# Kernel tuning notes

Measured on AMD Instinct MI355X. Metric: run time of the kernel, lower is better.

Reference implementation:

```python
import jax, jax.numpy as jnp
import numpy as np

G = 4        # split_group
H = 64       # hidden_size_t = 256 // 4 (causal -> //1)
I = 64       # input_size_t  = 256 // 4
EPS = 1e-5


def _lstm(x, W_ih, W_hh, b):
    """Grouped unidirectional LSTM, PyTorch gate order (i,f,g,o).
    x: (G,B,T,I); W_ih: (G,4H,I); W_hh: (G,4H,H); b: (G,4H) -> (G,B,T,H)"""
    g, bsz, t, _ = x.shape
    h_dim = W_hh.shape[-1]
    # precompute input projections for all timesteps
    xp = jnp.einsum('gbti,gki->gbtk', x, W_ih) + b[:, None, None, :]  # (G,B,T,4H)
    xp = jnp.moveaxis(xp, 2, 0)  # (T,G,B,4H)

    def step(carry, xt):
        h, c = carry
        gates = xt + jnp.einsum('gbh,gkh->gbk', h, W_hh)
        i_g, f_g, g_g, o_g = jnp.split(gates, 4, axis=-1)
        i_g = jax.nn.sigmoid(i_g)
        f_g = jax.nn.sigmoid(f_g)
        g_g = jnp.tanh(g_g)
        o_g = jax.nn.sigmoid(o_g)
        c = f_g * c + i_g * g_g
        h = o_g * jnp.tanh(c)
        return (h, c), h

    h0 = jnp.zeros((g, bsz, h_dim), x.dtype)
    _, hs = jax.lax.scan(step, (h0, h0), xp)  # hs: (T,G,B,H)
    return jnp.moveaxis(hs, 0, 2)  # (G,B,T,H)


def _bn(x, gamma, beta):
    """BatchNorm1d (training stats) over (B,T) per feature. x: (B,T,F)"""
    mean = x.mean(axis=(0, 1))
    var = x.var(axis=(0, 1))
    return (x - mean) * jax.lax.rsqrt(var + EPS) * gamma + beta


def setup_inputs() -> dict:
    key = jax.random.key(0)
    ks = jax.random.split(key, 12)
    s = 0.1
    F = G * H
    return {
        'inpt': jax.random.normal(ks[0], (32, 1000, 256), jnp.float32),
        'W_ih1': jax.random.normal(ks[1], (G, 4 * H, I), jnp.float32) * s,
        'W_hh1': jax.random.normal(ks[2], (G, 4 * H, H), jnp.float32) * s,
        'b1': jax.random.normal(ks[3], (G, 4 * H), jnp.float32) * s,
        'W_ih2': jax.random.normal(ks[4], (G, 4 * H, H), jnp.float32) * s,
        'W_hh2': jax.random.normal(ks[5], (G, 4 * H, H), jnp.float32) * s,
        'b2': jax.random.normal(ks[6], (G, 4 * H), jnp.float32) * s,
        'gamma1': jnp.ones((F,), jnp.float32) + jax.random.normal(ks[7], (F,)) * 0.01,
        'beta1': jax.random.normal(ks[8], (F,), jnp.float32) * 0.01,
        'gamma2': jnp.ones((F,), jnp.float32) + jax.random.normal(ks[9], (F,)) * 0.01,
        'beta2': jax.random.normal(ks[10], (F,), jnp.float32) * 0.01,
    }


def reference(inpt, W_ih1, W_hh1, b1, W_ih2, W_hh2, b2, gamma1, beta1, gamma2, beta2):
    B, T, F = inpt.shape
    # chunk along features -> (G,B,T,I)
    xg = jnp.transpose(inpt.reshape(B, T, G, I), (2, 0, 1, 3))
    y1 = _lstm(xg, W_ih1, W_hh1, b1)  # (G,B,T,H)
    # torch.stack(dim=-1) + flatten: feature index = h*G + g (interleaved)
    x = jnp.transpose(y1, (1, 2, 3, 0)).reshape(B, T, H * G)
    x = _bn(x, gamma1, beta1)
    # chunk again into G contiguous groups of size H
    xg2 = jnp.transpose(x.reshape(B, T, G, H), (2, 0, 1, 3))
    y2 = _lstm(xg2, W_ih2, W_hh2, b2)  # (G,B,T,H)
    # torch.cat(dim=-1): contiguous groups
    x = jnp.transpose(y2, (1, 2, 0, 3)).reshape(B, T, G * H)
    x = _bn(x, gamma2, beta2)
    return x
```

## Files before the change

### kernel.cpp

```cpp
#include <hip/hip_runtime.h>
#include <math.h>

#define G 4
#define H 64
#define T 1000
#define B 32
#define ROWS (B*T)

typedef _Float16 f16;
typedef _Float16 f16x2 __attribute__((ext_vector_type(2)));

#if defined(__has_builtin)
#if __has_builtin(__builtin_amdgcn_fdot2)
#define HAVE_FDOT2 1
#endif
#endif

__device__ __forceinline__ float dot2(f16x2 a, f16x2 b, float c) {
#ifdef HAVE_FDOT2
    return __builtin_amdgcn_fdot2(a, b, c, false);
#else
    return fmaf((float)a[0], (float)b[0], fmaf((float)a[1], (float)b[1], c));
#endif
}

__device__ __forceinline__ float sigm(float x) {
    return 1.f / (1.f + __expf(-x));
}
__device__ __forceinline__ float tanh_f(float x) {
    return 2.f / (1.f + __expf(-2.f * x)) - 1.f;
}

template<int LAYER>
__device__ void rec_wave4(const float* __restrict__ xp,
                          const float* __restrict__ Whh,
                          float* __restrict__ out,
                          float* __restrict__ stateh, float* __restrict__ statec,
                          float* __restrict__ sums,
                          int t0, int t1, int tcmax)
{
    __builtin_amdgcn_s_setprio(1);
    __shared__ __align__(16) _Float16 hx[4][64];
    const int wv = threadIdx.x >> 6;
    const int c  = threadIdx.x & 63;
    const int sq = blockIdx.x * 4 + wv;
    const int g = sq >> 5, b = sq & 31;

    f16x2 wpk[4][32];
    #pragma unroll
    for (int gt = 0; gt < 4; ++gt) {
        const float2* wp = (const float2*)&Whh[(size_t)((g * 256 + gt * 64 + c) << 6)];
        #pragma unroll
        for (int k = 0; k < 32; ++k) {
            float2 v = wp[k];
            f16x2 r; r[0] = (f16)v.x; r[1] = (f16)v.y;
            wpk[gt][k] = r;
        }
    }

    f16x2 hpk[32];
    float cst;
    if (t0 == 0) {
        #pragma unroll
        for (int k = 0; k < 32; ++k) { f16x2 z; z[0] = (f16)0.f; z[1] = (f16)0.f; hpk[k] = z; }
        cst = 0.f;
    } else {
        const float2* sh = (const float2*)&stateh[sq * 64];
        #pragma unroll
        for (int k = 0; k < 32; ++k) {
            float2 v = sh[k];
            f16x2 r; r[0] = (f16)v.x; r[1] = (f16)v.y;
            hpk[k] = r;
        }
        cst = statec[sq * 64 + c];
    }

    const float* xpb = xp + (size_t)sq * tcmax * 256;
    float p[4][4];
    #pragma unroll
    for (int j = 0; j < 4; ++j) {
        int tp = t0 + j; if (tp > t1 - 1) tp = t1 - 1;
        #pragma unroll
        for (int gt = 0; gt < 4; ++gt)
            p[j][gt] = xpb[(size_t)(tp - t0) * 256 + gt * 64 + c];
    }

    float st_s = 0.f, st_ss = 0.f, hl = 0.f;
    const int nsteps = t1 - t0;
    for (int s4 = 0; s4 < nsteps; s4 += 4) {
        #pragma unroll
        for (int j = 0; j < 4; ++j) {
            float pre[4];
            #pragma unroll
            for (int gt = 0; gt < 4; ++gt) {
                float a0 = 0.f, a1 = 0.f;
                #pragma unroll
                for (int k = 0; k < 32; k += 2) {
                    a0 = dot2(wpk[gt][k],     hpk[k],     a0);
                    a1 = dot2(wpk[gt][k + 1], hpk[k + 1], a1);
                }
                pre[gt] = (a0 + a1) + p[j][gt];
            }
            {
                int tp = t0 + s4 + j + 4; if (tp > t1 - 1) tp = t1 - 1;
                #pragma unroll
                for (int gt = 0; gt < 4; ++gt)
                    p[j][gt] = xpb[(size_t)(tp - t0) * 256 + gt * 64 + c];
            }
            float ig = sigm(pre[0]);
            float fg = sigm(pre[1]);
            float gg = tanh_f(pre[2]);
            float og = sigm(pre[3]);
            cst = fmaf(fg, cst, ig * gg);
            float h = og * tanh_f(cst);
            int t = t0 + s4 + j;
            if (LAYER == 1) out[((size_t)b * T + t) * 256 + c * 4 + g] = h;
            else            out[((size_t)b * T + t) * 256 + g * 64 + c] = h;
            st_s += h;
            st_ss = fmaf(h, h, st_ss);
            hl = h;
            hx[wv][c] = (f16)h;
            const float4* hp = (const float4*)&hx[wv][0];
            #pragma unroll
            for (int q = 0; q < 8; ++q) {
                float4 v = hp[q];
                hpk[q * 4 + 0] = __builtin_bit_cast(f16x2, v.x);
                hpk[q * 4 + 1] = __builtin_bit_cast(f16x2, v.y);
                hpk[q * 4 + 2] = __builtin_bit_cast(f16x2, v.z);
                hpk[q * 4 + 3] = __builtin_bit_cast(f16x2, v.w);
            }
        }
    }
    stateh[sq * 64 + c] = hl;
    statec[sq * 64 + c] = cst;
    int f = (LAYER == 1) ? (c * 4 + g) : (g * 64 + c);
    atomicAdd(&sums[f], st_s);
    atomicAdd(&sums[256 + f], st_ss);
}

template<bool BN>
__device__ void proj_tile(int id,
                          const float* __restrict__ xin,
                          const float* __restrict__ Wih,
                          const float* __restrict__ bias,
                          const float* __restrict__ ac,
                          float* __restrict__ xp,
                          int t0, int tcn, int tcmax, int TT)
{
    __shared__ __align__(16) float xs[64][68];
    __shared__ __align__(16) float wsm[64][68];

    const int tt = id % TT; id /= TT;
    const int b = id & 31;
    const int g = id >> 5;
    const int tid = threadIdx.x;
    const int tx = tid & 15, ty = tid >> 4;

    #pragma unroll
    for (int j = 0; j < 4; ++j) {
        int idx = j * 1024 + tid * 4;
        int r = idx >> 6, ci = idx & 63;
        int tg = t0 + tt * 64 + r; if (tg > T - 1) tg = T - 1;
        float4 v = *(const float4*)&xin[((size_t)b * T + tg) * 256 + g * 64 + ci];
        if (BN) {
            float4 a4 = *(const float4*)&ac[g * 64 + ci];
            float4 c4 = *(const float4*)&ac[256 + g * 64 + ci];
            v.x = fmaf(v.x, a4.x, c4.x);
            v.y = fmaf(v.y, a4.y, c4.y);
            v.z = fmaf(v.z, a4.z, c4.z);
            v.w = fmaf(v.w, a4.w, c4.w);
        }
        *(float4*)&xs[r][ci] = v;
    }

    float* xpb = xp + (size_t)(g * 32 + b) * tcmax * 256;

    for (int kt = 0; kt < 4; ++kt) {
        __syncthreads();
        #pragma unroll
        for (int j = 0; j < 4; ++j) {
            int idx = j * 1024 + tid * 4;
            int r = idx >> 6, ci = idx & 63;
            float4 v = *(const float4*)&Wih[(size_t)((g * 256 + kt * 64 + r) << 6) + ci];
            *(float4*)&wsm[r][ci] = v;
        }
        __syncthreads();

        float acc[4][4] = {};
        #pragma unroll
        for (int i4 = 0; i4 < 16; ++i4) {
            float4 xv[4], wv[4];
            #pragma unroll
            for (int q = 0; q < 4; ++q) xv[q] = *(const float4*)&xs[ty * 4 + q][i4 * 4];
            #pragma unroll
            for (int q = 0; q < 4; ++q) wv[q] = *(const float4*)&wsm[tx + 16 * q][i4 * 4];
            #pragma unroll
            for (int a = 0; a < 4; ++a)
                #pragma unroll
                for (int q = 0; q < 4; ++q) {
                    acc[a][q] = fmaf(xv[a].x, wv[q].x, acc[a][q]);
                    acc[a][q] = fmaf(xv[a].y, wv[q].y, acc[a][q]);
                    acc[a][q] = fmaf(xv[a].z, wv[q].z, acc[a][q]);
                    acc[a][q] = fmaf(xv[a].w, wv[q].w, acc[a][q]);
                }
        }

        float bq[4];
        #pragma unroll
        for (int q = 0; q < 4; ++q) bq[q] = bias[g * 256 + kt * 64 + tx + 16 * q];
        #pragma unroll
        for (int a = 0; a < 4; ++a) {
            int tloc = tt * 64 + ty * 4 + a;
            if (tloc < tcn) {
                #pragma unroll
                for (int q = 0; q < 4; ++q)
                    xpb[(size_t)tloc * 256 + kt * 64 + tx + 16 * q] = acc[a][q] + bq[q];
            }
        }
    }
}

template<int LAYER, bool PBN>
__global__ __launch_bounds__(256, 1)
void fused3(const float* __restrict__ xpA, const float* __restrict__ Whh,
            float* __restrict__ out,
            float* __restrict__ stateh, float* __restrict__ statec,
            float* __restrict__ sums,
            int t0, int t1, int tcmax,
            const float* __restrict__ xin, const float* __restrict__ Wih,
            const float* __restrict__ bias, const float* __restrict__ acbn,
            float* __restrict__ xpB, int t0n, int tcnn, int TTn)
{
    if (blockIdx.x < 32) {
        rec_wave4<LAYER>(xpA, Whh, out, stateh, statec, sums, t0, t1, tcmax);
    } else {
        proj_tile<PBN>(blockIdx.x - 32, xin, Wih, bias, acbn, xpB,
                       t0n, tcnn, tcmax, TTn);
    }
}

template<bool BN>
__global__ __launch_bounds__(256)
void xp_proj(const float* __restrict__ xin, const float* __restrict__ Wih,
             const float* __restrict__ bias, const float* __restrict__ ac,
             float* __restrict__ xp, int t0, int tcn, int tcmax, int TT)
{
    proj_tile<BN>(blockIdx.x, xin, Wih, bias, ac, xp, t0, tcn, tcmax, TT);
}

template<int LAYER>
__global__ __launch_bounds__(256, 1)
void rec_kernel(const float* __restrict__ xin,
                const float* __restrict__ Wih,
                const float* __restrict__ Whh,
                const float* __restrict__ bias,
                const float* __restrict__ bnac,
                float* __restrict__ out)
{
    const int g = blockIdx.x & 3;
    const int b = blockIdx.x >> 2;
    const int k = threadIdx.x;

    __shared__ __align__(16) float xsh[2][64];
    __shared__ __align__(16) float hsh[64];
    __shared__ __align__(16) float gsh[256];

    float wih[64], whh[64];
    {
        const float4* wi = (const float4*)(Wih + (size_t)(g * 256 + k) * 64);
        const float4* wh = (const float4*)(Whh + (size_t)(g * 256 + k) * 64);
        #pragma unroll
        for (int i = 0; i < 16; ++i) {
            float4 v = wi[i];
            wih[4*i] = v.x; wih[4*i+1] = v.y; wih[4*i+2] = v.z; wih[4*i+3] = v.w;
            float4 u = wh[i];
            whh[4*i] = u.x; whh[4*i+1] = u.y; whh[4*i+2] = u.z; whh[4*i+3] = u.w;
        }
    }
    const float bk = bias[g * 256 + k];
    const long rowbase = (long)b * T;
    const int  colbase = g * 64;

    float c = 0.f, af = 1.f, cf = 0.f;
    float xa = 0.f, xb = 0.f;

    if (k < 64) {
        if (LAYER == 2) { af = bnac[colbase + k]; cf = bnac[256 + colbase + k]; }
        hsh[k] = 0.f;
        float x0 = xin[(rowbase + 0) * 256 + colbase + k];
        xsh[0][k] = (LAYER == 2) ? fmaf(x0, af, cf) : x0;
        xa = xin[(rowbase + 1) * 256 + colbase + k];
        xb = xin[(rowbase + 2) * 256 + colbase + k];
    }
    __syncthreads();

    for (int t = 0; t < T; ++t) {
        const int cur = t & 1;
        float xn = 0.f;
        if (k < 64) {
            int tp = t + 3; if (tp > T - 1) tp = T - 1;
            xn = xin[(rowbase + tp) * 256 + colbase + k];
        }
        const float* xs = xsh[cur];
        float a0 = 0.f, a1 = 0.f, a2 = 0.f, a3 = 0.f;
        #pragma unroll
        for (int i = 0; i < 64; i += 4) {
            a0 = fmaf(wih[i],     xs[i],     a0);
            a1 = fmaf(wih[i + 1], xs[i + 1], a1);
            a2 = fmaf(wih[i + 2], xs[i + 2], a2);
            a3 = fmaf(wih[i + 3], xs[i + 3], a3);
        }
        #pragma unroll
        for (int jq = 0; jq < 64; jq += 4) {
            a0 = fmaf(whh[jq],     hsh[jq],     a0);
            a1 = fmaf(whh[jq + 1], hsh[jq + 1], a1);
            a2 = fmaf(whh[jq + 2], hsh[jq + 2], a2);
            a3 = fmaf(whh[jq + 3], hsh[jq + 3], a3);
        }
        const float acc = bk + ((a0 + a1) + (a2 + a3));
        const float act = (k >= 128 && k < 192) ? tanh_f(acc) : sigm(acc);
        gsh[k] = act;
        __syncthreads();

        if (k < 64) {
            const float ig = gsh[k];
            const float fg = gsh[64 + k];
            const float gg = gsh[128 + k];
            const float og = gsh[192 + k];
            c = fmaf(fg, c, ig * gg);
            const float h = og * tanh_f(c);
            hsh[k] = h;
            const long rrow = rowbase + t;
            if (LAYER == 1) out[rrow * 256 + k * 4 + g] = h;
            else            out[rrow * 256 + colbase + k] = h;
            xsh[cur ^ 1][k] = fmaf(xa, af, cf);
            xa = xb; xb = xn;
        }
        __syncthreads();
    }
}

__global__ void zero_ws(float* sums, int n) {
    int i = blockIdx.x * blockDim.x + threadIdx.x;
    if (i < n) sums[i] = 0.f;
}

__global__ __launch_bounds__(256) void stats_reduce(const float* __restrict__ x,
                                                    float* __restrict__ sums)
{
    float s = 0.f, ss = 0.f;
    for (int r = blockIdx.x; r < ROWS; r += gridDim.x) {
        float v = x[(long)r * 256 + threadIdx.x];
        s += v;
        ss = fmaf(v, v, ss);
    }
    atomicAdd(&sums[threadIdx.x], s);
    atomicAdd(&sums[256 + threadIdx.x], ss);
}

__global__ void stats_finalize(const float* __restrict__ sums,
                               const float* __restrict__ gamma,
                               const float* __restrict__ beta,
                               float* __restrict__ ac)
{
    int f = threadIdx.x;
    const float invN = 1.f / (float)ROWS;
    float mean = sums[f] * invN;
    float var  = fmaf(-mean, mean, sums[256 + f] * invN);
    float a = gamma[f] * rsqrtf(var + 1e-5f);
    ac[f]       = a;
    ac[256 + f] = fmaf(-mean, a, beta[f]);
}

__global__ __launch_bounds__(256) void bn_apply(float* __restrict__ x,
                                                const float* __restrict__ ac)
{
    __shared__ float a_s[256], c_s[256];
    a_s[threadIdx.x] = ac[threadIdx.x];
    c_s[threadIdx.x] = ac[256 + threadIdx.x];
    __syncthreads();
    const long n4 = (long)ROWS * 64;
    for (long i = (long)blockIdx.x * blockDim.x + threadIdx.x; i < n4;
         i += (long)gridDim.x * blockDim.x) {
        float4 v = ((float4*)x)[i];
        int f0 = (int)((i * 4) & 255);
        v.x = fmaf(v.x, a_s[f0],     c_s[f0]);
        v.y = fmaf(v.y, a_s[f0 + 1], c_s[f0 + 1]);
        v.z = fmaf(v.z, a_s[f0 + 2], c_s[f0 + 2]);
        v.w = fmaf(v.w, a_s[f0 + 3], c_s[f0 + 3]);
        ((float4*)x)[i] = v;
    }
}

extern "C" void kernel_launch(void* const* d_in, const int* in_sizes, int n_in,
                              void* d_out, int out_size, void* d_ws, size_t ws_size,
                              hipStream_t stream)
{
    const float* inpt   = (const float*)d_in[0];
    const float* Wih1   = (const float*)d_in[1];
    const float* Whh1   = (const float*)d_in[2];
    const float* b1     = (const float*)d_in[3];
    const float* Wih2   = (const float*)d_in[4];
    const float* Whh2   = (const float*)d_in[5];
    const float* b2     = (const float*)d_in[6];
    const float* gamma1 = (const float*)d_in[7];
    const float* beta1  = (const float*)d_in[8];
    const float* gamma2 = (const float*)d_in[9];
    const float* beta2  = (const float*)d_in[10];
    float* out  = (float*)d_out;

    float* sums1 = (float*)d_ws;
    float* sums2 = sums1 + 512;
    float* acbn1 = sums2 + 512;
    float* acbn2 = acbn1 + 512;
    float* sth   = acbn2 + 512;
    float* stc   = sth + 8192;
    float* xpb   = stc + 8192;

    const size_t fixedB = (size_t)(4 * 512 + 2 * 8192) * 4;
    const long perT = 128L * 256L * 4L;
    long availPair = ((long)ws_size - (long)fixedB) / (2L * perT);
    int Tc = (availPair >= 500) ? 500 : (int)(availPair & ~3L);

    if (Tc >= 8) {
        float* buf[2] = { xpb, xpb + (size_t)Tc * 128 * 256 };
        const int nch = (T + Tc - 1) / Tc;
        zero_ws<<<4, 256, 0, stream>>>(sums1, 1024);

        {
            int tcn0 = (Tc < T) ? Tc : T;
            int TT0 = (tcn0 + 63) / 64;
            xp_proj<false><<<128 * TT0, 256, 0, stream>>>(
                inpt, Wih1, b1, nullptr, buf[0], 0, tcn0, Tc, TT0);
            for (int c = 0; c < nch; ++c) {
                int t0 = c * Tc;
                int t1 = t0 + Tc; if (t1 > T) t1 = T;
                int t0n = t1;
                int tcnn = (c + 1 < nch) ? ((T - t0n < Tc) ? (T - t0n) : Tc) : 0;
                int TTn = (tcnn + 63) / 64;
                int grid = 32 + 128 * TTn;
                fused3<1, false><<<grid, 256, 0, stream>>>(
                    buf[c & 1], Whh1, out, sth, stc, sums1, t0, t1, Tc,
                    inpt, Wih1, b1, nullptr, buf[(c + 1) & 1], t0n, tcnn, TTn);
            }
        }
        stats_finalize<<<1, 256, 0, stream>>>(sums1, gamma1, beta1, acbn1);

        {
            int tcn0 = (Tc < T) ? Tc : T;
            int TT0 = (tcn0 + 63) / 64;
            xp_proj<true><<<128 * TT0, 256, 0, stream>>>(
                out, Wih2, b2, acbn1, buf[0], 0, tcn0, Tc, TT0);
            for (int c = 0; c < nch; ++c) {
                int t0 = c * Tc;
                int t1 = t0 + Tc; if (t1 > T) t1 = T;
                int t0n = t1;
                int tcnn = (c + 1 < nch) ? ((T - t0n < Tc) ? (T - t0n) : Tc) : 0;
                int TTn = (tcnn + 63) / 64;
                int grid = 32 + 128 * TTn;
                fused3<2, true><<<grid, 256, 0, stream>>>(
                    buf[c & 1], Whh2, out, sth, stc, sums2, t0, t1, Tc,
                    out, Wih2, b2, acbn1, buf[(c + 1) & 1], t0n, tcnn, TTn);
            }
        }
        stats_finalize<<<1, 256, 0, stream>>>(sums2, gamma2, beta2, acbn2);
        bn_apply<<<2048, 256, 0, stream>>>(out, acbn2);
    } else {
        zero_ws<<<2, 256, 0, stream>>>(sums1, 512);
        rec_kernel<1><<<G * B, 256, 0, stream>>>(inpt, Wih1, Whh1, b1, nullptr, out);
        stats_reduce<<<256, 256, 0, stream>>>(out, sums1);
        stats_finalize<<<1, 256, 0, stream>>>(sums1, gamma1, beta1, acbn1);
        rec_kernel<2><<<G * B, 256, 0, stream>>>(out, Wih2, Whh2, b2, acbn1, out);
        zero_ws<<<2, 256, 0, stream>>>(sums2, 512);
        stats_reduce<<<256, 256, 0, stream>>>(out, sums2);
        stats_finalize<<<1, 256, 0, stream>>>(sums2, gamma2, beta2, acbn2);
        bn_apply<<<2048, 256, 0, stream>>>(out, acbn2);
    }
}
```

Measured before the change: 1.473 ms.

## Process two batch sequences per wave and use uneven chunk schedule

Each recurrent wave now advances two independent (group,batch) sequences at once, reusing the same register-resident W_hh weights. This halves the recurrent blocks from 32 to 16 and interleaves two independent dot-product and activation chains to hide latency. The time chunking also changes to a short first chunk (128) followed by two 436-step chunks, so the serial pre-projection before the first recurrence is shorter. The cost is more registers per thread and twice the serial work per wave, which could lengthen the critical path if the extra parallelism does not hide latency.

```diff
diff --git a/kernel.cpp b/kernel.cpp
--- a/kernel.cpp
+++ b/kernel.cpp
@@ -32,7 +32,7 @@
 }
 
 template<int LAYER>
-__device__ void rec_wave4(const float* __restrict__ xp,
+__device__ void rec_wave2(const float* __restrict__ xp,
                           const float* __restrict__ Whh,
                           float* __restrict__ out,
                           float* __restrict__ stateh, float* __restrict__ statec,
@@ -40,11 +40,13 @@
                           int t0, int t1, int tcmax)
 {
     __builtin_amdgcn_s_setprio(1);
-    __shared__ __align__(16) _Float16 hx[4][64];
+    __shared__ __align__(16) _Float16 hx[4][2][64];
     const int wv = threadIdx.x >> 6;
     const int c  = threadIdx.x & 63;
-    const int sq = blockIdx.x * 4 + wv;
-    const int g = sq >> 5, b = sq & 31;
+    const int Wid = blockIdx.x * 4 + wv;
+    const int g = Wid >> 4, b = Wid & 15;
+    const int sqA = g * 32 + b;
+    const int sqB = sqA + 16;
 
     f16x2 wpk[4][32];
     #pragma unroll
@@ -58,84 +60,114 @@
         }
     }
 
-    f16x2 hpk[32];
-    float cst;
+    f16x2 hA[32], hB[32];
+    float cA, cB;
     if (t0 == 0) {
         #pragma unroll
-        for (int k = 0; k < 32; ++k) { f16x2 z; z[0] = (f16)0.f; z[1] = (f16)0.f; hpk[k] = z; }
-        cst = 0.f;
+        for (int k = 0; k < 32; ++k) {
+            f16x2 z; z[0] = (f16)0.f; z[1] = (f16)0.f;
+            hA[k] = z; hB[k] = z;
+        }
+        cA = 0.f; cB = 0.f;
     } else {
-        const float2* sh = (const float2*)&stateh[sq * 64];
+        const float2* shA = (const float2*)&stateh[sqA * 64];
+        const float2* shB = (const float2*)&stateh[sqB * 64];
         #pragma unroll
         for (int k = 0; k < 32; ++k) {
-            float2 v = sh[k];
-            f16x2 r; r[0] = (f16)v.x; r[1] = (f16)v.y;
-            hpk[k] = r;
-        }
-        cst = statec[sq * 64 + c];
-    }
-
-    const float* xpb = xp + (size_t)sq * tcmax * 256;
-    float p[4][4];
+            float2 va = shA[k], vb = shB[k];
+            f16x2 ra; ra[0] = (f16)va.x; ra[1] = (f16)va.y;
+            f16x2 rb; rb[0] = (f16)vb.x; rb[1] = (f16)vb.y;
+            hA[k] = ra; hB[k] = rb;
+        }
+        cA = statec[sqA * 64 + c];
+        cB = statec[sqB * 64 + c];
+    }
+
+    const float* xpA = xp + (size_t)sqA * tcmax * 256;
+    const float* xpB = xp + (size_t)sqB * tcmax * 256;
+    float pA[2][4], pB[2][4];
     #pragma unroll
-    for (int j = 0; j < 4; ++j) {
+    for (int j = 0; j < 2; ++j) {
         int tp = t0 + j; if (tp > t1 - 1) tp = t1 - 1;
         #pragma unroll
-        for (int gt = 0; gt < 4; ++gt)
-            p[j][gt] = xpb[(size_t)(tp - t0) * 256 + gt * 64 + c];
-    }
-
-    float st_s = 0.f, st_ss = 0.f, hl = 0.f;
+        for (int gt = 0; gt < 4; ++gt) {
+            pA[j][gt] = xpA[(size_t)(tp - t0) * 256 + gt * 64 + c];
+            pB[j][gt] = xpB[(size_t)(tp - t0) * 256 + gt * 64 + c];
+        }
+    }
+
+    float sA = 0.f, ssA = 0.f, hlA = 0.f;
+    float sB = 0.f, ssB = 0.f, hlB = 0.f;
     const int nsteps = t1 - t0;
-    for (int s4 = 0; s4 < nsteps; s4 += 4) {
-        #pragma unroll
-        for (int j = 0; j < 4; ++j) {
-            float pre[4];
+    for (int s2 = 0; s2 < nsteps; s2 += 2) {
+        #pragma unroll
+        for (int j = 0; j < 2; ++j) {
+            float preA[4], preB[4];
             #pragma unroll
             for (int gt = 0; gt < 4; ++gt) {
-                float a0 = 0.f, a1 = 0.f;
+                float a0 = 0.f, a1 = 0.f, b0 = 0.f, b1 = 0.f;
                 #pragma unroll
                 for (int k = 0; k < 32; k += 2) {
-                    a0 = dot2(wpk[gt][k],     hpk[k],     a0);
-                    a1 = dot2(wpk[gt][k + 1], hpk[k + 1], a1);
+                    a0 = dot2(wpk[gt][k],     hA[k],     a0);
+                    b0 = dot2(wpk[gt][k],     hB[k],     b0);
+                    a1 = dot2(wpk[gt][k + 1], hA[k + 1], a1);
+                    b1 = dot2(wpk[gt][k + 1], hB[k + 1], b1);
                 }
-                pre[gt] = (a0 + a1) + p[j][gt];
+                preA[gt] = (a0 + a1) + pA[j][gt];
+                preB[gt] = (b0 + b1) + pB[j][gt];
             }
             {
-                int tp = t0 + s4 + j + 4; if (tp > t1 - 1) tp = t1 - 1;
+                int tp = t0 + s2 + j + 2; if (tp > t1 - 1) tp = t1 - 1;
                 #pragma unroll
-                for (int gt = 0; gt < 4; ++gt)
-                    p[j][gt] = xpb[(size_t)(tp - t0) * 256 + gt * 64 + c];
+                for (int gt = 0; gt < 4; ++gt) {
+                    pA[j][gt] = xpA[(size_t)(tp - t0) * 256 + gt * 64 + c];
+                    pB[j][gt] = xpB[(size_t)(tp - t0) * 256 + gt * 64 + c];
+                }
             }
-            float ig = sigm(pre[0]);
-            float fg = sigm(pre[1]);
-            float gg = tanh_f(pre[2]);
-            float og = sigm(pre[3]);
-            cst = fmaf(fg, cst, ig * gg);
-            float h = og * tanh_f(cst);
-            int t = t0 + s4 + j;
-            if (LAYER == 1) out[((size_t)b * T + t) * 256 + c * 4 + g] = h;
-            else            out[((size_t)b * T + t) * 256 + g * 64 + c] = h;
-            st_s += h;
-            st_ss = fmaf(h, h, st_ss);
-            hl = h;
-            hx[wv][c] = (f16)h;
-            const float4* hp = (const float4*)&hx[wv][0];
+            float igA = sigm(preA[0]), igB = sigm(preB[0]);
+            float fgA = sigm(preA[1]), fgB = sigm(preB[1]);
+            float ggA = tanh_f(preA[2]), ggB = tanh_f(preB[2]);
+            float ogA = sigm(preA[3]), ogB = sigm(preB[3]);
+            cA = fmaf(fgA, cA, igA * ggA);
+            cB = fmaf(fgB, cB, igB * ggB);
+            float hAv = ogA * tanh_f(cA);
+            float hBv = ogB * tanh_f(cB);
+            int t = t0 + s2 + j;
+            if (LAYER == 1) {
+                out[((size_t)b * T + t) * 256 + c * 4 + g] = hAv;
+                out[((size_t)(b + 16) * T + t) * 256 + c * 4 + g] = hBv;
+            } else {
+                out[((size_t)b * T + t) * 256 + g * 64 + c] = hAv;
+                out[((size_t)(b + 16) * T + t) * 256 + g * 64 + c] = hBv;
+            }
+            sA += hAv; ssA = fmaf(hAv, hAv, ssA); hlA = hAv;
+            sB += hBv; ssB = fmaf(hBv, hBv, ssB); hlB = hBv;
+            hx[wv][0][c] = (f16)hAv;
+            hx[wv][1][c] = (f16)hBv;
+            const float4* rpA = (const float4*)&hx[wv][0][0];
+            const float4* rpB = (const float4*)&hx[wv][1][0];
             #pragma unroll
             for (int q = 0; q < 8; ++q) {
-                float4 v = hp[q];
-                hpk[q * 4 + 0] = __builtin_bit_cast(f16x2, v.x);
-                hpk[q * 4 + 1] = __builtin_bit_cast(f16x2, v.y);
-                hpk[q * 4 + 2] = __builtin_bit_cast(f16x2, v.z);
-                hpk[q * 4 + 3] = __builtin_bit_cast(f16x2, v.w);
+                float4 va = rpA[q];
+                float4 vb = rpB[q];
+                hA[q * 4 + 0] = __builtin_bit_cast(f16x2, va.x);
+                hA[q * 4 + 1] = __builtin_bit_cast(f16x2, va.y);
+                hA[q * 4 + 2] = __builtin_bit_cast(f16x2, va.z);
+                hA[q * 4 + 3] = __builtin_bit_cast(f16x2, va.w);
+                hB[q * 4 + 0] = __builtin_bit_cast(f16x2, vb.x);
+                hB[q * 4 + 1] = __builtin_bit_cast(f16x2, vb.y);
+                hB[q * 4 + 2] = __builtin_bit_cast(f16x2, vb.z);
+                hB[q * 4 + 3] = __builtin_bit_cast(f16x2, vb.w);
             }
         }
     }
-    stateh[sq * 64 + c] = hl;
-    statec[sq * 64 + c] = cst;
+    stateh[sqA * 64 + c] = hlA;
+    stateh[sqB * 64 + c] = hlB;
+    statec[sqA * 64 + c] = cA;
+    statec[sqB * 64 + c] = cB;
     int f = (LAYER == 1) ? (c * 4 + g) : (g * 64 + c);
-    atomicAdd(&sums[f], st_s);
-    atomicAdd(&sums[256 + f], st_ss);
+    atomicAdd(&sums[f], sA + sB);
+    atomicAdd(&sums[256 + f], ssA + ssB);
 }
 
 template<bool BN>
@@ -231,10 +263,10 @@
             const float* __restrict__ bias, const float* __restrict__ acbn,
             float* __restrict__ xpB, int t0n, int tcnn, int TTn)
 {
-    if (blockIdx.x < 32) {
-        rec_wave4<LAYER>(xpA, Whh, out, stateh, statec, sums, t0, t1, tcmax);
+    if (blockIdx.x < 16) {
+        rec_wave2<LAYER>(xpA, Whh, out, stateh, statec, sums, t0, t1, tcmax);
     } else {
-        proj_tile<PBN>(blockIdx.x - 32, xin, Wih, bias, acbn, xpB,
+        proj_tile<PBN>(blockIdx.x - 16, xin, Wih, bias, acbn, xpB,
                        t0n, tcnn, tcmax, TTn);
     }
 }
@@ -420,50 +452,63 @@
     const size_t fixedB = (size_t)(4 * 512 + 2 * 8192) * 4;
     const long perT = 128L * 256L * 4L;
     long availPair = ((long)ws_size - (long)fixedB) / (2L * perT);
-    int Tc = (availPair >= 500) ? 500 : (int)(availPair & ~3L);
-
-    if (Tc >= 8) {
-        float* buf[2] = { xpb, xpb + (size_t)Tc * 128 * 256 };
-        const int nch = (T + Tc - 1) / Tc;
+
+    int chunks[8]; int nch = 0;
+    if (availPair >= 436) {
+        chunks[0] = 128; chunks[1] = 436; chunks[2] = 436; nch = 3;
+    } else if (availPair >= 8) {
+        int Tc = (int)(availPair & ~3L);
+        int acc = 0;
+        while (acc < T && nch < 8) {
+            int c = T - acc; if (c > Tc) c = Tc;
+            chunks[nch++] = c; acc += c;
+        }
+        if (acc < T) nch = 0;
+    }
+
+    if (nch > 0) {
+        int tcmax = 0;
+        for (int i = 0; i < nch; ++i) if (chunks[i] > tcmax) tcmax = chunks[i];
+        float* buf[2] = { xpb, xpb + (size_t)tcmax * 128 * 256 };
         zero_ws<<<4, 256, 0, stream>>>(sums1, 1024);
 
-        {
-            int tcn0 = (Tc < T) ? Tc : T;
-            int TT0 = (tcn0 + 63) / 64;
-            xp_proj<false><<<128 * TT0, 256, 0, stream>>>(
-                inpt, Wih1, b1, nullptr, buf[0], 0, tcn0, Tc, TT0);
+        for (int layer = 1; layer <= 2; ++layer) {
+            const float* xin  = (layer == 1) ? inpt : out;
+            const float* Wih  = (layer == 1) ? Wih1 : Wih2;
+            const float* Whh  = (layer == 1) ? Whh1 : Whh2;
+            const float* bb   = (layer == 1) ? b1 : b2;
+            float* sums       = (layer == 1) ? sums1 : sums2;
+
+            int t0 = 0;
+            int TT0 = (chunks[0] + 63) / 64;
+            if (layer == 1)
+                xp_proj<false><<<128 * TT0, 256, 0, stream>>>(
+                    xin, Wih, bb, nullptr, buf[0], 0, chunks[0], tcmax, TT0);
+            else
+                xp_proj<true><<<128 * TT0, 256, 0, stream>>>(
+                    xin, Wih, bb, acbn1, buf[0], 0, chunks[0], tcmax, TT0);
+
             for (int c = 0; c < nch; ++c) {
-                int t0 = c * Tc;
-                int t1 = t0 + Tc; if (t1 > T) t1 = T;
+                int t1 = t0 + chunks[c];
                 int t0n = t1;
-                int tcnn = (c + 1 < nch) ? ((T - t0n < Tc) ? (T - t0n) : Tc) : 0;
+                int tcnn = (c + 1 < nch) ? chunks[c + 1] : 0;
                 int TTn = (tcnn + 63) / 64;
-                int grid = 32 + 128 * TTn;
-                fused3<1, false><<<grid, 256, 0, stream>>>(
-                    buf[c & 1], Whh1, out, sth, stc, sums1, t0, t1, Tc,
-                    inpt, Wih1, b1, nullptr, buf[(c + 1) & 1], t0n, tcnn, TTn);
+                int grid = 16 + 128 * TTn;
+                if (layer == 1)
+                    fused3<1, false><<<grid, 256, 0, stream>>>(
+                        buf[c & 1], Whh, out, sth, stc, sums, t0, t1, tcmax,
+                        xin, Wih, bb, nullptr, buf[(c + 1) & 1], t0n, tcnn, TTn);
+                else
+                    fused3<2, true><<<grid, 256, 0, stream>>>(
+                        buf[c & 1], Whh, out, sth, stc, sums, t0, t1, tcmax,
+                        xin, Wih, bb, acbn1, buf[(c + 1) & 1], t0n, tcnn, TTn);
+                t0 = t1;
             }
-        }
-        stats_finalize<<<1, 256, 0, stream>>>(sums1, gamma1, beta1, acbn1);
-
-        {
-            int tcn0 = (Tc < T) ? Tc : T;
-            int TT0 = (tcn0 + 63) / 64;
-            xp_proj<true><<<128 * TT0, 256, 0, stream>>>(
-                out, Wih2, b2, acbn1, buf[0], 0, tcn0, Tc, TT0);
-            for (int c = 0; c < nch; ++c) {
-                int t0 = c * Tc;
-                int t1 = t0 + Tc; if (t1 > T) t1 = T;
-                int t0n = t1;
-                int tcnn = (c + 1 < nch) ? ((T - t0n < Tc) ? (T - t0n) : Tc) : 0;
-                int TTn = (tcnn + 63) / 64;
-                int grid = 32 + 128 * TTn;
-                fused3<2, true><<<grid, 256, 0, stream>>>(
-                    buf[c & 1], Whh2, out, sth, stc, sums2, t0, t1, Tc,
-                    out, Wih2, b2, acbn1, buf[(c + 1) & 1], t0n, tcnn, TTn);
-            }
-        }
-        stats_finalize<<<1, 256, 0, stream>>>(sums2, gamma2, beta2, acbn2);
+            if (layer == 1)
+                stats_finalize<<<1, 256, 0, stream>>>(sums1, gamma1, beta1, acbn1);
+            else
+                stats_finalize<<<1, 256, 0, stream>>>(sums2, gamma2, beta2, acbn2);
+        }
         bn_apply<<<2048, 256, 0, stream>>>(out, acbn2);
     } else {
         zero_ws<<<2, 256, 0, stream>>>(sums1, 512);
```

Result: slower. 2.074 ms (+40.8%).

## Stage LSTM input projections via async global-to-LDS double buffer and rebalance chunks

Applied to the files above, without the earlier changes.

The recurrent loop now prefetches groups of eight timesteps of precomputed input projections straight into LDS with global_load_lds, double-buffered, instead of holding four register-prefetched timesteps per lane. This aims to take global-load latency and register pressure out of the serial recurrence. The host side also replaces equal 500-step chunks with uneven chunks (128, 440, 432), so the first projection kernel, which nothing overlaps, is smaller. Costs are extra LDS, a full vmcnt wait per group, and the requirement that every chunk length be a multiple of eight.

```diff
diff --git a/kernel.cpp b/kernel.cpp
--- a/kernel.cpp
+++ b/kernel.cpp
@@ -6,6 +6,7 @@
 #define T 1000
 #define B 32
 #define ROWS (B*T)
+#define SS 8
 
 typedef _Float16 f16;
 typedef _Float16 f16x2 __attribute__((ext_vector_type(2)));
@@ -30,6 +31,9 @@
 __device__ __forceinline__ float tanh_f(float x) {
     return 2.f / (1.f + __expf(-2.f * x)) - 1.f;
 }
+
+typedef const __attribute__((address_space(1))) void gas_void;
+typedef __attribute__((address_space(3))) void las_void;
 
 template<int LAYER>
 __device__ void rec_wave4(const float* __restrict__ xp,
@@ -40,6 +44,7 @@
                           int t0, int t1, int tcmax)
 {
     __builtin_amdgcn_s_setprio(1);
+    __shared__ __align__(16) float xbuf[2][SS][4][256];
     __shared__ __align__(16) _Float16 hx[4][64];
     const int wv = threadIdx.x >> 6;
     const int c  = threadIdx.x & 63;
@@ -76,36 +81,72 @@
     }
 
     const float* xpb = xp + (size_t)sq * tcmax * 256;
-    float p[4][4];
+
     #pragma unroll
-    for (int j = 0; j < 4; ++j) {
-        int tp = t0 + j; if (tp > t1 - 1) tp = t1 - 1;
-        #pragma unroll
-        for (int gt = 0; gt < 4; ++gt)
-            p[j][gt] = xpb[(size_t)(tp - t0) * 256 + gt * 64 + c];
-    }
+    for (int j = 0; j < SS; ++j) {
+        const float* gsrc = xpb + (size_t)j * 256 + c * 4;
+        __builtin_amdgcn_global_load_lds((gas_void*)gsrc,
+                                         (las_void*)&xbuf[0][j][wv][0], 16, 0, 0);
+    }
+    asm volatile("s_waitcnt vmcnt(0)" ::: "memory");
+    __builtin_amdgcn_sched_barrier(0);
 
     float st_s = 0.f, st_ss = 0.f, hl = 0.f;
-    const int nsteps = t1 - t0;
-    for (int s4 = 0; s4 < nsteps; s4 += 4) {
-        #pragma unroll
-        for (int j = 0; j < 4; ++j) {
+    const int ngrp = (t1 - t0) / SS;
+    for (int grp = 0; grp < ngrp; ++grp) {
+        const int cur = grp & 1;
+        if (grp + 1 < ngrp) {
+            const int lbase = (grp + 1) * SS;
+            #pragma unroll
+            for (int j = 0; j < SS; ++j) {
+                const float* gsrc = xpb + (size_t)(lbase + j) * 256 + c * 4;
+                __builtin_amdgcn_global_load_lds((gas_void*)gsrc,
+                                                 (las_void*)&xbuf[cur ^ 1][j][wv][0],
+                                                 16, 0, 0);
+            }
+        }
+        #pragma unroll
+        for (int j = 0; j < SS; ++j) {
+            float pj0 = xbuf[cur][j][wv][c];
+            float pj1 = xbuf[cur][j][wv][64 + c];
+            float pj2 = xbuf[cur][j][wv][128 + c];
+            float pj3 = xbuf[cur][j][wv][192 + c];
             float pre[4];
-            #pragma unroll
-            for (int gt = 0; gt < 4; ++gt) {
+            {
                 float a0 = 0.f, a1 = 0.f;
                 #pragma unroll
                 for (int k = 0; k < 32; k += 2) {
-                    a0 = dot2(wpk[gt][k],     hpk[k],     a0);
-                    a1 = dot2(wpk[gt][k + 1], hpk[k + 1], a1);
+                    a0 = dot2(wpk[0][k],     hpk[k],     a0);
+                    a1 = dot2(wpk[0][k + 1], hpk[k + 1], a1);
                 }
-                pre[gt] = (a0 + a1) + p[j][gt];
+                pre[0] = (a0 + a1) + pj0;
             }
             {
-                int tp = t0 + s4 + j + 4; if (tp > t1 - 1) tp = t1 - 1;
+                float a0 = 0.f, a1 = 0.f;
                 #pragma unroll
-                for (int gt = 0; gt < 4; ++gt)
-                    p[j][gt] = xpb[(size_t)(tp - t0) * 256 + gt * 64 + c];
+                for (int k = 0; k < 32; k += 2) {
+                    a0 = dot2(wpk[1][k],     hpk[k],     a0);
+                    a1 = dot2(wpk[1][k + 1], hpk[k + 1], a1);
+                }
+                pre[1] = (a0 + a1) + pj1;
+            }
+            {
+                float a0 = 0.f, a1 = 0.f;
+                #pragma unroll
+                for (int k = 0; k < 32; k += 2) {
+                    a0 = dot2(wpk[2][k],     hpk[k],     a0);
+                    a1 = dot2(wpk[2][k + 1], hpk[k + 1], a1);
+                }
+                pre[2] = (a0 + a1) + pj2;
+            }
+            {
+                float a0 = 0.f, a1 = 0.f;
+                #pragma unroll
+                for (int k = 0; k < 32; k += 2) {
+                    a0 = dot2(wpk[3][k],     hpk[k],     a0);
+                    a1 = dot2(wpk[3][k + 1], hpk[k + 1], a1);
+                }
+                pre[3] = (a0 + a1) + pj3;
             }
             float ig = sigm(pre[0]);
             float fg = sigm(pre[1]);
@@ -113,7 +154,7 @@
             float og = sigm(pre[3]);
             cst = fmaf(fg, cst, ig * gg);
             float h = og * tanh_f(cst);
-            int t = t0 + s4 + j;
+            int t = t0 + grp * SS + j;
             if (LAYER == 1) out[((size_t)b * T + t) * 256 + c * 4 + g] = h;
             else            out[((size_t)b * T + t) * 256 + g * 64 + c] = h;
             st_s += h;
@@ -130,6 +171,8 @@
                 hpk[q * 4 + 3] = __builtin_bit_cast(f16x2, v.w);
             }
         }
+        asm volatile("s_waitcnt vmcnt(0)" ::: "memory");
+        __builtin_amdgcn_sched_barrier(0);
     }
     stateh[sq * 64 + c] = hl;
     statec[sq * 64 + c] = cst;
@@ -420,50 +463,63 @@
     const size_t fixedB = (size_t)(4 * 512 + 2 * 8192) * 4;
     const long perT = 128L * 256L * 4L;
     long availPair = ((long)ws_size - (long)fixedB) / (2L * perT);
-    int Tc = (availPair >= 500) ? 500 : (int)(availPair & ~3L);
-
-    if (Tc >= 8) {
-        float* buf[2] = { xpb, xpb + (size_t)Tc * 128 * 256 };
-        const int nch = (T + Tc - 1) / Tc;
+
+    int chunks[8]; int nch = 0;
+    if (availPair >= 440) {
+        chunks[0] = 128; chunks[1] = 440; chunks[2] = 432; nch = 3;
+    } else if (availPair >= SS) {
+        int Tc = (int)(availPair & ~(long)(SS - 1));
+        int acc = 0;
+        while (acc < T && nch < 8) {
+            int c = T - acc; if (c > Tc) c = Tc;
+            chunks[nch++] = c; acc += c;
+        }
+        if (acc < T) nch = 0;
+    }
+
+    if (nch > 0) {
+        int tcmax = 0;
+        for (int i = 0; i < nch; ++i) if (chunks[i] > tcmax) tcmax = chunks[i];
+        float* buf[2] = { xpb, xpb + (size_t)tcmax * 128 * 256 };
         zero_ws<<<4, 256, 0, stream>>>(sums1, 1024);
 
-        {
-            int tcn0 = (Tc < T) ? Tc : T;
-            int TT0 = (tcn0 + 63) / 64;
-            xp_proj<false><<<128 * TT0, 256, 0, stream>>>(
-                inpt, Wih1, b1, nullptr, buf[0], 0, tcn0, Tc, TT0);
+        for (int layer = 1; layer <= 2; ++layer) {
+            const float* xin  = (layer == 1) ? inpt : out;
+            const float* Wih  = (layer == 1) ? Wih1 : Wih2;
+            const float* Whh  = (layer == 1) ? Whh1 : Whh2;
+            const float* bb   = (layer == 1) ? b1 : b2;
+            float* sums       = (layer == 1) ? sums1 : sums2;
+
+            int t0 = 0;
+            int TT0 = (chunks[0] + 63) / 64;
+            if (layer == 1)
+                xp_proj<false><<<128 * TT0, 256, 0, stream>>>(
+                    xin, Wih, bb, nullptr, buf[0], 0, chunks[0], tcmax, TT0);
+            else
+                xp_proj<true><<<128 * TT0, 256, 0, stream>>>(
+                    xin, Wih, bb, acbn1, buf[0], 0, chunks[0], tcmax, TT0);
+
             for (int c = 0; c < nch; ++c) {
-                int t0 = c * Tc;
-                int t1 = t0 + Tc; if (t1 > T) t1 = T;
+                int t1 = t0 + chunks[c];
                 int t0n = t1;
-                int tcnn = (c + 1 < nch) ? ((T - t0n < Tc) ? (T - t0n) : Tc) : 0;
+                int tcnn = (c + 1 < nch) ? chunks[c + 1] : 0;
                 int TTn = (tcnn + 63) / 64;
                 int grid = 32 + 128 * TTn;
-                fused3<1, false><<<grid, 256, 0, stream>>>(
-                    buf[c & 1], Whh1, out, sth, stc, sums1, t0, t1, Tc,
-                    inpt, Wih1, b1, nullptr, buf[(c + 1) & 1], t0n, tcnn, TTn);
-            }
-        }
-        stats_finalize<<<1, 256, 0, stream>>>(sums1, gamma1, beta1, acbn1);
-
-        {
-            int tcn0 = (Tc < T) ? Tc : T;
-            int TT0 = (tcn0 + 63) / 64;
-            xp_proj<true><<<128 * TT0, 256, 0, stream>>>(
-                out, Wih2, b2, acbn1, buf[0], 0, tcn0, Tc, TT0);
-            for (int c = 0; c < nch; ++c) {
-                int t0 = c * Tc;
-                int t1 = t0 + Tc; if (t1 > T) t1 = T;
-                int t0n = t1;
-                int tcnn = (c + 1 < nch) ? ((T - t0n < Tc) ? (T - t0n) : Tc) : 0;
-                int TTn = (tcnn + 63) / 64;
-                int grid = 32 + 128 * TTn;
-                fused3<2, true><<<grid, 256, 0, stream>>>(
-                    buf[c & 1], Whh2, out, sth, stc, sums2, t0, t1, Tc,
-                    out, Wih2, b2, acbn1, buf[(c + 1) & 1], t0n, tcnn, TTn);
-            }
-        }
-        stats_finalize<<<1, 256, 0, stream>>>(sums2, gamma2, beta2, acbn2);
+                if (layer == 1)
+                    fused3<1, false><<<grid, 256, 0, stream>>>(
+                        buf[c & 1], Whh, out, sth, stc, sums, t0, t1, tcmax,
+                        xin, Wih, bb, nullptr, buf[(c + 1) & 1], t0n, tcnn, TTn);
+                else
+                    fused3<2, true><<<grid, 256, 0, stream>>>(
+                        buf[c & 1], Whh, out, sth, stc, sums, t0, t1, tcmax,
+                        xin, Wih, bb, acbn1, buf[(c + 1) & 1], t0n, tcnn, TTn);
+                t0 = t1;
+            }
+            if (layer == 1)
+                stats_finalize<<<1, 256, 0, stream>>>(sums1, gamma1, beta1, acbn1);
+            else
+                stats_finalize<<<1, 256, 0, stream>>>(sums2, gamma2, beta2, acbn2);
+        }
         bn_apply<<<2048, 256, 0, stream>>>(out, acbn2);
     } else {
         zero_ws<<<2, 256, 0, stream>>>(sums1, 512);
```

Measured after the change: 1.379 ms. 6.3% less time.
